# Kernel optimization log

Measured on AMD Instinct MI355X. Metric: run time of the kernel, lower is better.

Reference implementation:

```python
import jax, jax.numpy as jnp
import numpy as np

TOP_K = 2
NUM_EXPERTS = 8
ROUTE_SCALE = 1.0


def setup_inputs() -> dict:
    key = jax.random.key(0)
    ks = jax.random.split(key, 8)
    bs, slen, dim, hidden, E = 4, 1024, 2048, 1024, NUM_EXPERTS
    s = 0.02
    return {
        "x": jax.random.normal(ks[0], (bs, slen, dim), jnp.float32),
        "gate_w": jax.random.normal(ks[1], (E, dim), jnp.float32) * s,
        "w1": jax.random.normal(ks[2], (E, hidden, dim), jnp.float32) * s,
        "w2": jax.random.normal(ks[3], (E, dim, hidden), jnp.float32) * s,
        "w3": jax.random.normal(ks[4], (E, hidden, dim), jnp.float32) * s,
        "ws1": jax.random.normal(ks[5], (hidden, dim), jnp.float32) * s,
        "ws2": jax.random.normal(ks[6], (dim, hidden), jnp.float32) * s,
        "ws3": jax.random.normal(ks[7], (hidden, dim), jnp.float32) * s,
    }


def reference(x, gate_w, w1, w2, w3, ws1, ws2, ws3):
    bs, slen, dim = x.shape
    xf = x.reshape(-1, dim)  # (T, dim)
    # --- router: sigmoid scores in fp32, top-k (expert_bias is zeros at init) ---
    logits = (xf @ gate_w.T).astype(jnp.float32)  # (T, E)
    scores = jax.nn.sigmoid(logits)
    top_scores, sel_idx = jax.lax.top_k(scores, TOP_K)  # (T, k), (T, k)
    top_scores = top_scores * ROUTE_SCALE  # route_norm=False
    # --- routed experts: score_before_experts=True -> scale input by score ---
    routed = jnp.zeros_like(xf)
    for k in range(TOP_K):
        xs = xf * top_scores[:, k][:, None]  # (T, dim)
        h1 = jnp.einsum('td,ehd->teh', xs, w1)
        h3 = jnp.einsum('td,ehd->teh', xs, w3)
        h = jax.nn.silu(h1) * h3  # (T, E, hidden)
        onehot = jax.nn.one_hot(sel_idx[:, k], NUM_EXPERTS, dtype=h.dtype)  # (T, E)
        routed = routed + jnp.einsum('teh,te,edh->td', h, onehot, w2)
    # --- shared expert (SwiGLU FFN) ---
    shared = (jax.nn.silu(xf @ ws1.T) * (xf @ ws3.T)) @ ws2.T
    out = (shared + routed).reshape(bs, slen, dim)
    return out
```

## Files before the change

kernel.cpp:

```cpp
#include <hip/hip_runtime.h>
#include <hip/hip_bf16.h>
#include <cstdint>

#define TTOK   4096
#define DIM    2048
#define HID    1024
#define NEXP   8
#define GROWS  12288

typedef __attribute__((ext_vector_type(8))) __bf16 bf16x8;
typedef __attribute__((ext_vector_type(4))) float  f32x4;

__device__ __forceinline__ void glds16(const void* g, void* l) {
  __builtin_amdgcn_global_load_lds((const __attribute__((address_space(1))) void*)g,
                                   (__attribute__((address_space(3))) void*)l,
                                   16, 0, 0);
}

__global__ void convert_w(const float* __restrict__ w1, const float* __restrict__ w2,
                          const float* __restrict__ w3, const float* __restrict__ ws1,
                          const float* __restrict__ ws2, const float* __restrict__ ws3,
                          __bf16* __restrict__ w13, __bf16* __restrict__ w2c) {
  const int N1 = 9 * 2048 * 2048 / 8;
  const int N2 = 9 * 2048 * 1024 / 8;
  int s = blockIdx.x * 256 + threadIdx.x;
  const float* src;
  __bf16* dst;
  if (s < N1) {
    int e  = s / 524288;
    int r  = (s % 524288) / 256;
    int c  = (s % 256) * 8;
    if (r < 1024) src = (e < 8 ? w1 + ((size_t)e * 1024 + r) * 2048 : ws1 + (size_t)r * 2048) + c;
    else          src = (e < 8 ? w3 + ((size_t)e * 1024 + (r - 1024)) * 2048 : ws3 + (size_t)(r - 1024) * 2048) + c;
    dst = w13 + ((size_t)e * 2048 + r) * 2048 + c;
  } else {
    int s2 = s - N1;
    if (s2 >= N2) return;
    int e  = s2 / 262144;
    int r  = (s2 % 262144) / 128;
    int c  = (s2 % 128) * 8;
    src = (e < 8 ? w2 + ((size_t)e * 2048 + r) * 1024 : ws2 + (size_t)r * 1024) + c;
    dst = w2c + ((size_t)e * 2048 + r) * 1024 + c;
  }
  float4 a = *(const float4*)(src);
  float4 b = *(const float4*)(src + 4);
  bf16x8 o;
  o[0]=(__bf16)a.x; o[1]=(__bf16)a.y; o[2]=(__bf16)a.z; o[3]=(__bf16)a.w;
  o[4]=(__bf16)b.x; o[5]=(__bf16)b.y; o[6]=(__bf16)b.z; o[7]=(__bf16)b.w;
  *(bf16x8*)dst = o;
}

__global__ void router_k(const float* __restrict__ x, const float* __restrict__ gw,
                         int* __restrict__ sel, float* __restrict__ sco, int* __restrict__ counts) {
  int t    = blockIdx.x * 4 + (threadIdx.x >> 6);
  int lane = threadIdx.x & 63;
  const float* xr = x + (size_t)t * DIM;
  float acc[NEXP];
  #pragma unroll
  for (int e = 0; e < NEXP; ++e) acc[e] = 0.f;
  for (int d = lane * 4; d < DIM; d += 256) {
    float4 xv = *(const float4*)(xr + d);
    #pragma unroll
    for (int e = 0; e < NEXP; ++e) {
      float4 gv = *(const float4*)(gw + (size_t)e * DIM + d);
      acc[e] += xv.x * gv.x + xv.y * gv.y + xv.z * gv.z + xv.w * gv.w;
    }
  }
  #pragma unroll
  for (int off = 32; off; off >>= 1)
    #pragma unroll
    for (int e = 0; e < NEXP; ++e) acc[e] += __shfl_xor(acc[e], off);
  if (lane == 0) {
    float s[NEXP];
    #pragma unroll
    for (int e = 0; e < NEXP; ++e) s[e] = 1.f / (1.f + expf(-acc[e]));
    int e0 = 0;
    #pragma unroll
    for (int e = 1; e < NEXP; ++e) if (s[e] > s[e0]) e0 = e;
    int e1 = (e0 == 0) ? 1 : 0;
    #pragma unroll
    for (int e = 0; e < NEXP; ++e) if (e != e0 && s[e] > s[e1]) e1 = e;
    sel[2 * t] = e0; sel[2 * t + 1] = e1;
    sco[2 * t] = s[e0]; sco[2 * t + 1] = s[e1];
    atomicAdd(&counts[e0], 1); atomicAdd(&counts[e1], 1);
  }
}

__global__ void scan_k(const int* __restrict__ counts, int* __restrict__ offs) {
  if (threadIdx.x == 0 && blockIdx.x == 0) {
    int o = 0;
    for (int e = 0; e < NEXP; ++e) { offs[e] = o; o += counts[e]; }
    offs[NEXP] = o;
    offs[NEXP + 1] = o + TTOK;
  }
}

__global__ void gather_k(const float* __restrict__ x, const int* __restrict__ sel,
                         const float* __restrict__ sco, const int* __restrict__ offs,
                         int* __restrict__ cursor, int* __restrict__ token_rows,
                         __bf16* __restrict__ xg) {
  __shared__ int   rows[3];
  __shared__ float ss[3];
  int t = blockIdx.x;
  if (threadIdx.x == 0) {
    int e0 = sel[2 * t], e1 = sel[2 * t + 1];
    int r0 = offs[e0] + atomicAdd(&cursor[e0], 1);
    int r1 = offs[e1] + atomicAdd(&cursor[e1], 1);
    int r2 = 8192 + t;
    rows[0] = r0; rows[1] = r1; rows[2] = r2;
    ss[0] = sco[2 * t]; ss[1] = sco[2 * t + 1]; ss[2] = 1.0f;
    token_rows[3 * t] = r0; token_rows[3 * t + 1] = r1; token_rows[3 * t + 2] = r2;
  }
  __syncthreads();
  int c = threadIdx.x * 8;
  float4 v0 = *(const float4*)(x + (size_t)t * DIM + c);
  float4 v1 = *(const float4*)(x + (size_t)t * DIM + c + 4);
  #pragma unroll
  for (int j = 0; j < 3; ++j) {
    float s = ss[j];
    bf16x8 o;
    o[0]=(__bf16)(v0.x*s); o[1]=(__bf16)(v0.y*s); o[2]=(__bf16)(v0.z*s); o[3]=(__bf16)(v0.w*s);
    o[4]=(__bf16)(v1.x*s); o[5]=(__bf16)(v1.y*s); o[6]=(__bf16)(v1.z*s); o[7]=(__bf16)(v1.w*s);
    *(bf16x8*)(xg + (size_t)rows[j] * DIM + c) = o;
  }
}

template <int EPI>
__launch_bounds__(256)
__global__ void gemm_nt(const __bf16* __restrict__ A, const __bf16* __restrict__ Bw,
                        __bf16* __restrict__ Cb, float* __restrict__ c2a, float* __restrict__ c2b,
                        const int* __restrict__ offs, int K_, int N_) {
  int z  = blockIdx.z;
  int o0 = offs[z];
  int ne = offs[z + 1] - o0;

  int flat = blockIdx.y * 32 + blockIdx.x;
  int nid  = (flat & 7) * 64 + (flat >> 3);
  int bm   = nid & 31;
  int bn   = nid >> 5;

  if (bm * 128 >= ne) return;

  const __bf16* Aseg = A  + (size_t)(o0 + bm * 128) * K_;
  const __bf16* Bseg = Bw + ((size_t)z * N_ + bn * 128) * K_;

  __shared__ __align__(16) __bf16 sA[2][128 * 64];
  __shared__ __align__(16) __bf16 sB[2][128 * 64];

  int tid  = threadIdx.x;
  int wave = tid >> 6, lane = tid & 63;
  int wm = wave & 1, wn = wave >> 1;
  int fr = lane & 15;
  int fq = lane >> 4;
  int sw = fr & 7;

  f32x4 acc[4][4];
  #pragma unroll
  for (int i = 0; i < 4; ++i)
    #pragma unroll
    for (int j = 0; j < 4; ++j) acc[i][j] = (f32x4){0.f, 0.f, 0.f, 0.f};

#define STAGE(buf, kbase)                                                     \
  {                                                                           \
    _Pragma("unroll")                                                         \
    for (int it = 0; it < 4; ++it) {                                          \
      int s   = it * 256 + tid;                                               \
      int row = s >> 3;                                                       \
      int c8  = (s & 7) ^ (row & 7);                                          \
      glds16(Aseg + (size_t)row * K_ + (kbase) + c8 * 8, &sA[buf][s * 8]);    \
      glds16(Bseg + (size_t)row * K_ + (kbase) + c8 * 8, &sB[buf][s * 8]);    \
    }                                                                         \
  }

  STAGE(0, 0)
  __syncthreads();

  const int nk = K_ >> 6;
  for (int t = 0; t < nk; ++t) {
    int cur = t & 1;
    if (t + 1 < nk) STAGE(cur ^ 1, (t + 1) << 6)

    const __bf16* rAbase = &sA[cur][(wm * 64 + fr) * 64];
    const __bf16* rBbase = &sB[cur][(wn * 64 + fr) * 64];
    #pragma unroll
    for (int kk = 0; kk < 2; ++kk) {
      int slot = ((kk * 4 + fq) ^ sw) * 8;
      bf16x8 af[4], bb[4];
      #pragma unroll
      for (int i = 0; i < 4; ++i) af[i] = *(const bf16x8*)(rAbase + i * 16 * 64 + slot);
      #pragma unroll
      for (int i = 0; i < 4; ++i) bb[i] = *(const bf16x8*)(rBbase + i * 16 * 64 + slot);
      #pragma unroll
      for (int mi = 0; mi < 4; ++mi)
        #pragma unroll
        for (int ni = 0; ni < 4; ++ni)
          acc[mi][ni] = __builtin_amdgcn_mfma_f32_16x16x32_bf16(af[mi], bb[ni], acc[mi][ni], 0, 0, 0);
    }
    __syncthreads();
  }
#undef STAGE

  #pragma unroll
  for (int mi = 0; mi < 4; ++mi) {
    #pragma unroll
    for (int r = 0; r < 4; ++r) {
      int rl = bm * 128 + wm * 64 + mi * 16 + fq * 4 + r;
      if (rl < ne) {
        int grow = o0 + rl;
        if (EPI == 0) {
          size_t ro = (size_t)grow * 2048;
          #pragma unroll
          for (int ni = 0; ni < 4; ++ni) {
            int col = bn * 128 + wn * 64 + ni * 16 + fr;
            Cb[ro + col] = (__bf16)acc[mi][ni][r];
          }
        } else {
          float* dst = (grow < 8192) ? (c2a + (size_t)grow * 2048)
                                     : (c2b + (size_t)(grow - 8192) * 2048);
          #pragma unroll
          for (int ni = 0; ni < 4; ++ni) {
            int col = bn * 128 + wn * 64 + ni * 16 + fr;
            dst[col] = acc[mi][ni][r];
          }
        }
      }
    }
  }
}

__global__ void silu_mul(const __bf16* __restrict__ c13, __bf16* __restrict__ h) {
  int i   = blockIdx.x * 256 + threadIdx.x;
  int row = i >> 7;
  int c   = (i & 127) * 8;
  bf16x8 a = *(const bf16x8*)(c13 + (size_t)row * 2048 + c);
  bf16x8 b = *(const bf16x8*)(c13 + (size_t)row * 2048 + 1024 + c);
  bf16x8 o;
  #pragma unroll
  for (int j = 0; j < 8; ++j) {
    float xv = (float)a[j];
    float g  = xv / (1.f + expf(-xv));
    o[j] = (__bf16)(g * (float)b[j]);
  }
  *(bf16x8*)(h + (size_t)row * 1024 + c) = o;
}

__global__ void combine_k(const float* __restrict__ c2a, const float* __restrict__ c2b,
                          const int* __restrict__ token_rows, float* __restrict__ out) {
  __shared__ int rr[3];
  int t = blockIdx.x;
  if (threadIdx.x < 3) rr[threadIdx.x] = token_rows[3 * t + threadIdx.x];
  __syncthreads();
  int c = threadIdx.x * 8;
  const float* p0 = c2a + (size_t)rr[0] * 2048 + c;
  const float* p1 = c2a + (size_t)rr[1] * 2048 + c;
  const float* p2 = c2b + (size_t)(rr[2] - 8192) * 2048 + c;
  float4 a0 = *(const float4*)p0,       a1 = *(const float4*)p1,       a2 = *(const float4*)p2;
  float4 b0 = *(const float4*)(p0 + 4), b1 = *(const float4*)(p1 + 4), b2 = *(const float4*)(p2 + 4);
  float4 oa, ob;
  oa.x = a0.x + a1.x + a2.x; oa.y = a0.y + a1.y + a2.y;
  oa.z = a0.z + a1.z + a2.z; oa.w = a0.w + a1.w + a2.w;
  ob.x = b0.x + b1.x + b2.x; ob.y = b0.y + b1.y + b2.y;
  ob.z = b0.z + b1.z + b2.z; ob.w = b0.w + b1.w + b2.w;
  float* op = out + (size_t)t * 2048 + c;
  *(float4*)op = oa;
  *(float4*)(op + 4) = ob;
}

extern "C" void kernel_launch(void* const* d_in, const int* in_sizes, int n_in,
                              void* d_out, int out_size, void* d_ws, size_t ws_size,
                              hipStream_t stream) {
  const float* x   = (const float*)d_in[0];
  const float* gw  = (const float*)d_in[1];
  const float* w1  = (const float*)d_in[2];
  const float* w2  = (const float*)d_in[3];
  const float* w3  = (const float*)d_in[4];
  const float* ws1 = (const float*)d_in[5];
  const float* ws2 = (const float*)d_in[6];
  const float* ws3 = (const float*)d_in[7];
  float* out = (float*)d_out;

  char* p = (char*)d_ws;
  int*   counts     = (int*)p;
  int*   cursor     = (int*)(p + 64);
  int*   offs       = (int*)(p + 128);
  int*   sel        = (int*)(p + 1024);
  float* sco        = (float*)(p + 1024 + 32768);
  int*   token_rows = (int*)(p + 1024 + 65536);
  char* big = p + (1 << 20);
  __bf16* w13 = (__bf16*)big;
  __bf16* w2c = (__bf16*)(big + 75497472ull);
  __bf16* xg  = (__bf16*)(big + 75497472ull + 37748736ull);
  __bf16* c13 = (__bf16*)(big + 75497472ull + 37748736ull + 50331648ull);
  __bf16* hbuf = xg;
  float*  c2a  = (float*)w13;
  float*  c2b  = (float*)c13;

  hipMemsetAsync(p, 0, 256, stream);

  convert_w<<<27648, 256, 0, stream>>>(w1, w2, w3, ws1, ws2, ws3, w13, w2c);
  router_k<<<TTOK / 4, 256, 0, stream>>>(x, gw, sel, sco, counts);
  scan_k<<<1, 64, 0, stream>>>(counts, offs);
  gather_k<<<TTOK, 256, 0, stream>>>(x, sel, sco, offs, cursor, token_rows, xg);
  gemm_nt<0><<<dim3(32, 16, 9), 256, 0, stream>>>(xg, w13, c13, nullptr, nullptr, offs, 2048, 2048);
  silu_mul<<<GROWS * HID / 8 / 256, 256, 0, stream>>>(c13, hbuf);
  gemm_nt<1><<<dim3(32, 16, 9), 256, 0, stream>>>(hbuf, w2c, nullptr, c2a, c2b, offs, 1024, 2048);
  combine_k<<<TTOK, 256, 0, stream>>>(c2a, c2b, token_rows, out);
}
```

Measured before the change: 751.5 us.

## Fuse SiLU-mul into gate/up GEMM epilogue and enlarge GEMM tiles to 256x256

Interleaves the w1 and w3 rows in the converted weights so that adjacent output columns hold the h1/h3 pair, letting the first grouped GEMM compute silu(h1)*h3 in its epilogue with a lane shuffle and write the hidden activations directly. This removes the separate silu_mul kernel and the full bf16 round trip of the intermediate c13 buffer. The GEMM is also retiled to 256x256 blocks with 512 threads, explicit vmcnt waits, raw barriers and s_setprio around the MFMA bursts to overlap loads with compute. The larger tiles double LDS use and raise register pressure, and they halve the block count for experts with few rows. The extra barriers inside the inner loop may also cost time.

Measured after the change: 778.2 us. +3.5%, slower.

```diff
diff --git a/kernel.cpp b/kernel.cpp
--- a/kernel.cpp
+++ b/kernel.cpp
@@ -16,6 +16,9 @@
                                    (__attribute__((address_space(3))) void*)l,
                                    16, 0, 0);
 }
+
+#define BAR() do { asm volatile("" ::: "memory"); __builtin_amdgcn_s_barrier(); \
+                   asm volatile("" ::: "memory"); } while (0)
 
 __global__ void convert_w(const float* __restrict__ w1, const float* __restrict__ w2,
                           const float* __restrict__ w3, const float* __restrict__ ws1,
@@ -30,9 +33,12 @@
     int e  = s / 524288;
     int r  = (s % 524288) / 256;
     int c  = (s % 256) * 8;
-    if (r < 1024) src = (e < 8 ? w1 + ((size_t)e * 1024 + r) * 2048 : ws1 + (size_t)r * 2048) + c;
-    else          src = (e < 8 ? w3 + ((size_t)e * 1024 + (r - 1024)) * 2048 : ws3 + (size_t)(r - 1024) * 2048) + c;
-    dst = w13 + ((size_t)e * 2048 + r) * 2048 + c;
+    int nr;
+    if (r < 1024) { src = (e < 8 ? w1 + ((size_t)e * 1024 + r) * 2048 : ws1 + (size_t)r * 2048) + c;
+                    nr = 2 * r; }
+    else          { src = (e < 8 ? w3 + ((size_t)e * 1024 + (r - 1024)) * 2048 : ws3 + (size_t)(r - 1024) * 2048) + c;
+                    nr = 2 * (r - 1024) + 1; }
+    dst = w13 + ((size_t)e * 2048 + nr) * 2048 + c;
   } else {
     int s2 = s - N1;
     if (s2 >= N2) return;
@@ -126,37 +132,38 @@
 }
 
 template <int EPI>
-__launch_bounds__(256)
+__launch_bounds__(512, 2)
 __global__ void gemm_nt(const __bf16* __restrict__ A, const __bf16* __restrict__ Bw,
-                        __bf16* __restrict__ Cb, float* __restrict__ c2a, float* __restrict__ c2b,
+                        __bf16* __restrict__ Hb, float* __restrict__ c2a, float* __restrict__ c2b,
                         const int* __restrict__ offs, int K_, int N_) {
   int z  = blockIdx.z;
   int o0 = offs[z];
   int ne = offs[z + 1] - o0;
 
-  int flat = blockIdx.y * 32 + blockIdx.x;
-  int nid  = (flat & 7) * 64 + (flat >> 3);
-  int bm   = nid & 31;
-  int bn   = nid >> 5;
-
-  if (bm * 128 >= ne) return;
-
-  const __bf16* Aseg = A  + (size_t)(o0 + bm * 128) * K_;
-  const __bf16* Bseg = Bw + ((size_t)z * N_ + bn * 128) * K_;
-
-  __shared__ __align__(16) __bf16 sA[2][128 * 64];
-  __shared__ __align__(16) __bf16 sB[2][128 * 64];
+  int flat = blockIdx.y * 16 + blockIdx.x;
+  int nid  = (flat & 7) * 16 + (flat >> 3);
+  int bm   = nid & 15;
+  int bn   = nid >> 4;
+
+  if (bm * 256 >= ne) return;
+
+  const __bf16* Aseg = A  + (size_t)(o0 + bm * 256) * K_;
+  const __bf16* Bseg = Bw + ((size_t)z * N_ + bn * 256) * K_;
+
+  __shared__ __align__(16) __bf16 sA[2][256 * 64];
+  __shared__ __align__(16) __bf16 sB[2][256 * 64];
 
   int tid  = threadIdx.x;
   int wave = tid >> 6, lane = tid & 63;
-  int wm = wave & 1, wn = wave >> 1;
+  int wm = wave & 1;
+  int wn = wave >> 1;
   int fr = lane & 15;
   int fq = lane >> 4;
   int sw = fr & 7;
 
-  f32x4 acc[4][4];
-  #pragma unroll
-  for (int i = 0; i < 4; ++i)
+  f32x4 acc[8][4];
+  #pragma unroll
+  for (int i = 0; i < 8; ++i)
     #pragma unroll
     for (int j = 0; j < 4; ++j) acc[i][j] = (f32x4){0.f, 0.f, 0.f, 0.f};
 
@@ -164,7 +171,7 @@
   {                                                                           \
     _Pragma("unroll")                                                         \
     for (int it = 0; it < 4; ++it) {                                          \
-      int s   = it * 256 + tid;                                               \
+      int s   = it * 512 + tid;                                               \
       int row = s >> 3;                                                       \
       int c8  = (s & 7) ^ (row & 7);                                          \
       glds16(Aseg + (size_t)row * K_ + (kbase) + c8 * 8, &sA[buf][s * 8]);    \
@@ -173,75 +180,83 @@
   }
 
   STAGE(0, 0)
-  __syncthreads();
+  asm volatile("s_waitcnt vmcnt(0)" ::: "memory");
+  BAR();
 
   const int nk = K_ >> 6;
   for (int t = 0; t < nk; ++t) {
     int cur = t & 1;
-    if (t + 1 < nk) STAGE(cur ^ 1, (t + 1) << 6)
-
-    const __bf16* rAbase = &sA[cur][(wm * 64 + fr) * 64];
-    const __bf16* rBbase = &sB[cur][(wn * 64 + fr) * 64];
+    if (t + 1 < nk) {
+      STAGE(cur ^ 1, (t + 1) << 6)
+      asm volatile("s_waitcnt vmcnt(8)" ::: "memory");
+    } else {
+      asm volatile("s_waitcnt vmcnt(0)" ::: "memory");
+    }
+    BAR();
+
+    const __bf16* sAc = &sA[cur][0];
+    const __bf16* sBc = &sB[cur][0];
     #pragma unroll
     for (int kk = 0; kk < 2; ++kk) {
       int slot = ((kk * 4 + fq) ^ sw) * 8;
-      bf16x8 af[4], bb[4];
+      bf16x8 bb[4];
       #pragma unroll
-      for (int i = 0; i < 4; ++i) af[i] = *(const bf16x8*)(rAbase + i * 16 * 64 + slot);
+      for (int i = 0; i < 4; ++i)
+        bb[i] = *(const bf16x8*)(sBc + (wn * 64 + i * 16 + fr) * 64 + slot);
       #pragma unroll
-      for (int i = 0; i < 4; ++i) bb[i] = *(const bf16x8*)(rBbase + i * 16 * 64 + slot);
-      #pragma unroll
-      for (int mi = 0; mi < 4; ++mi)
+      for (int mh = 0; mh < 2; ++mh) {
+        bf16x8 af[4];
         #pragma unroll
-        for (int ni = 0; ni < 4; ++ni)
-          acc[mi][ni] = __builtin_amdgcn_mfma_f32_16x16x32_bf16(af[mi], bb[ni], acc[mi][ni], 0, 0, 0);
+        for (int i = 0; i < 4; ++i)
+          af[i] = *(const bf16x8*)(sAc + (wm * 128 + (mh * 4 + i) * 16 + fr) * 64 + slot);
+        BAR();
+        __builtin_amdgcn_s_setprio(1);
+        #pragma unroll
+        for (int i = 0; i < 4; ++i)
+          #pragma unroll
+          for (int j = 0; j < 4; ++j)
+            acc[mh * 4 + i][j] =
+                __builtin_amdgcn_mfma_f32_16x16x32_bf16(af[i], bb[j], acc[mh * 4 + i][j], 0, 0, 0);
+        __builtin_amdgcn_s_setprio(0);
+        BAR();
+      }
     }
-    __syncthreads();
   }
 #undef STAGE
 
   #pragma unroll
-  for (int mi = 0; mi < 4; ++mi) {
+  for (int mi = 0; mi < 8; ++mi) {
     #pragma unroll
     for (int r = 0; r < 4; ++r) {
-      int rl = bm * 128 + wm * 64 + mi * 16 + fq * 4 + r;
-      if (rl < ne) {
-        int grow = o0 + rl;
-        if (EPI == 0) {
-          size_t ro = (size_t)grow * 2048;
-          #pragma unroll
-          for (int ni = 0; ni < 4; ++ni) {
-            int col = bn * 128 + wn * 64 + ni * 16 + fr;
-            Cb[ro + col] = (__bf16)acc[mi][ni][r];
+      int rl = bm * 256 + wm * 128 + mi * 16 + fq * 4 + r;
+      bool ok = rl < ne;
+      int grow = o0 + rl;
+      if (EPI == 0) {
+        #pragma unroll
+        for (int ni = 0; ni < 4; ++ni) {
+          float v = acc[mi][ni][r];
+          float o = __shfl_xor(v, 1);
+          float h1 = (fr & 1) ? o : v;
+          float h3 = (fr & 1) ? v : o;
+          float g  = h1 / (1.f + expf(-h1)) * h3;
+          if (ok && !(fr & 1)) {
+            int hcol = bn * 128 + wn * 32 + ni * 8 + (fr >> 1);
+            Hb[(size_t)grow * 1024 + hcol] = (__bf16)g;
           }
-        } else {
+        }
+      } else {
+        if (ok) {
           float* dst = (grow < 8192) ? (c2a + (size_t)grow * 2048)
                                      : (c2b + (size_t)(grow - 8192) * 2048);
           #pragma unroll
           for (int ni = 0; ni < 4; ++ni) {
-            int col = bn * 128 + wn * 64 + ni * 16 + fr;
+            int col = bn * 256 + wn * 64 + ni * 16 + fr;
             dst[col] = acc[mi][ni][r];
           }
         }
       }
     }
   }
-}
-
-__global__ void silu_mul(const __bf16* __restrict__ c13, __bf16* __restrict__ h) {
-  int i   = blockIdx.x * 256 + threadIdx.x;
-  int row = i >> 7;
-  int c   = (i & 127) * 8;
-  bf16x8 a = *(const bf16x8*)(c13 + (size_t)row * 2048 + c);
-  bf16x8 b = *(const bf16x8*)(c13 + (size_t)row * 2048 + 1024 + c);
-  bf16x8 o;
-  #pragma unroll
-  for (int j = 0; j < 8; ++j) {
-    float xv = (float)a[j];
-    float g  = xv / (1.f + expf(-xv));
-    o[j] = (__bf16)(g * (float)b[j]);
-  }
-  *(bf16x8*)(h + (size_t)row * 1024 + c) = o;
 }
 
 __global__ void combine_k(const float* __restrict__ c2a, const float* __restrict__ c2b,
@@ -287,13 +302,12 @@
   float* sco        = (float*)(p + 1024 + 32768);
   int*   token_rows = (int*)(p + 1024 + 65536);
   char* big = p + (1 << 20);
-  __bf16* w13 = (__bf16*)big;
-  __bf16* w2c = (__bf16*)(big + 75497472ull);
-  __bf16* xg  = (__bf16*)(big + 75497472ull + 37748736ull);
-  __bf16* c13 = (__bf16*)(big + 75497472ull + 37748736ull + 50331648ull);
-  __bf16* hbuf = xg;
+  __bf16* w13  = (__bf16*)big;
+  __bf16* w2c  = (__bf16*)(big + 75497472ull);
+  __bf16* xg   = (__bf16*)(big + 75497472ull + 37748736ull);
+  __bf16* hbuf = (__bf16*)(big + 75497472ull + 37748736ull + 50331648ull);
   float*  c2a  = (float*)w13;
-  float*  c2b  = (float*)c13;
+  float*  c2b  = (float*)xg;
 
   hipMemsetAsync(p, 0, 256, stream);
 
@@ -301,8 +315,7 @@
   router_k<<<TTOK / 4, 256, 0, stream>>>(x, gw, sel, sco, counts);
   scan_k<<<1, 64, 0, stream>>>(counts, offs);
   gather_k<<<TTOK, 256, 0, stream>>>(x, sel, sco, offs, cursor, token_rows, xg);
-  gemm_nt<0><<<dim3(32, 16, 9), 256, 0, stream>>>(xg, w13, c13, nullptr, nullptr, offs, 2048, 2048);
-  silu_mul<<<GROWS * HID / 8 / 256, 256, 0, stream>>>(c13, hbuf);
-  gemm_nt<1><<<dim3(32, 16, 9), 256, 0, stream>>>(hbuf, w2c, nullptr, c2a, c2b, offs, 1024, 2048);
+  gemm_nt<0><<<dim3(16, 8, 9), 512, 0, stream>>>(xg, w13, hbuf, nullptr, nullptr, offs, 2048, 2048);
+  gemm_nt<1><<<dim3(16, 8, 9), 512, 0, stream>>>(hbuf, w2c, nullptr, c2a, c2b, offs, 1024, 2048);
   combine_k<<<TTOK, 256, 0, stream>>>(c2a, c2b, token_rows, out);
 }
```

## Fuse SiLU-mul into gate/up GEMM epilogue via interleaved w1/w3 rows

Applied to the files above, without the earlier changes.

The weight conversion now interleaves w1 and w3 rows, so each adjacent pair of output columns in the first grouped GEMM holds matching h1 and h3 values. The epilogue swaps them with a lane shuffle, applies SiLU times gate, and writes the bf16 hidden activations directly. This removes the separate silu_mul pass and its bf16 c13 round trip through memory. Weight conversion and the router are also merged into a single launch to cut one kernel launch. In exchange, half the lanes issue scattered 2-byte stores, and c2b is now aliased onto xg, so buffer-reuse correctness depends on xg holding at least 4096 fp32 rows of 2048.

New measurement: 741.6 us. No clear change (-1.3%).

```diff
diff --git a/kernel.cpp b/kernel.cpp
--- a/kernel.cpp
+++ b/kernel.cpp
@@ -17,42 +17,49 @@
                                    16, 0, 0);
 }
 
-__global__ void convert_w(const float* __restrict__ w1, const float* __restrict__ w2,
-                          const float* __restrict__ w3, const float* __restrict__ ws1,
-                          const float* __restrict__ ws2, const float* __restrict__ ws3,
-                          __bf16* __restrict__ w13, __bf16* __restrict__ w2c) {
+__global__ void convert_router_k(const float* __restrict__ w1, const float* __restrict__ w2,
+                                 const float* __restrict__ w3, const float* __restrict__ ws1,
+                                 const float* __restrict__ ws2, const float* __restrict__ ws3,
+                                 __bf16* __restrict__ w13, __bf16* __restrict__ w2c,
+                                 const float* __restrict__ x, const float* __restrict__ gw,
+                                 int* __restrict__ sel, float* __restrict__ sco,
+                                 int* __restrict__ counts) {
   const int N1 = 9 * 2048 * 2048 / 8;
   const int N2 = 9 * 2048 * 1024 / 8;
-  int s = blockIdx.x * 256 + threadIdx.x;
-  const float* src;
-  __bf16* dst;
-  if (s < N1) {
-    int e  = s / 524288;
-    int r  = (s % 524288) / 256;
-    int c  = (s % 256) * 8;
-    if (r < 1024) src = (e < 8 ? w1 + ((size_t)e * 1024 + r) * 2048 : ws1 + (size_t)r * 2048) + c;
-    else          src = (e < 8 ? w3 + ((size_t)e * 1024 + (r - 1024)) * 2048 : ws3 + (size_t)(r - 1024) * 2048) + c;
-    dst = w13 + ((size_t)e * 2048 + r) * 2048 + c;
-  } else {
-    int s2 = s - N1;
-    if (s2 >= N2) return;
-    int e  = s2 / 262144;
-    int r  = (s2 % 262144) / 128;
-    int c  = (s2 % 128) * 8;
-    src = (e < 8 ? w2 + ((size_t)e * 2048 + r) * 1024 : ws2 + (size_t)r * 1024) + c;
-    dst = w2c + ((size_t)e * 2048 + r) * 1024 + c;
-  }
-  float4 a = *(const float4*)(src);
-  float4 b = *(const float4*)(src + 4);
-  bf16x8 o;
-  o[0]=(__bf16)a.x; o[1]=(__bf16)a.y; o[2]=(__bf16)a.z; o[3]=(__bf16)a.w;
-  o[4]=(__bf16)b.x; o[5]=(__bf16)b.y; o[6]=(__bf16)b.z; o[7]=(__bf16)b.w;
-  *(bf16x8*)dst = o;
-}
-
-__global__ void router_k(const float* __restrict__ x, const float* __restrict__ gw,
-                         int* __restrict__ sel, float* __restrict__ sco, int* __restrict__ counts) {
-  int t    = blockIdx.x * 4 + (threadIdx.x >> 6);
+  const int CONV_BLOCKS = (N1 + N2) / 256;
+
+  if (blockIdx.x < (unsigned)CONV_BLOCKS) {
+    int s = blockIdx.x * 256 + threadIdx.x;
+    const float* src;
+    __bf16* dst;
+    if (s < N1) {
+      int e  = s / 524288;
+      int r  = (s % 524288) / 256;
+      int c  = (s % 256) * 8;
+      int nr;
+      if (r < 1024) { src = (e < 8 ? w1 + ((size_t)e * 1024 + r) * 2048 : ws1 + (size_t)r * 2048) + c;
+                      nr = 2 * r; }
+      else          { src = (e < 8 ? w3 + ((size_t)e * 1024 + (r - 1024)) * 2048 : ws3 + (size_t)(r - 1024) * 2048) + c;
+                      nr = 2 * (r - 1024) + 1; }
+      dst = w13 + ((size_t)e * 2048 + nr) * 2048 + c;
+    } else {
+      int s2 = s - N1;
+      int e  = s2 / 262144;
+      int r  = (s2 % 262144) / 128;
+      int c  = (s2 % 128) * 8;
+      src = (e < 8 ? w2 + ((size_t)e * 2048 + r) * 1024 : ws2 + (size_t)r * 1024) + c;
+      dst = w2c + ((size_t)e * 2048 + r) * 1024 + c;
+    }
+    float4 a = *(const float4*)(src);
+    float4 b = *(const float4*)(src + 4);
+    bf16x8 o;
+    o[0]=(__bf16)a.x; o[1]=(__bf16)a.y; o[2]=(__bf16)a.z; o[3]=(__bf16)a.w;
+    o[4]=(__bf16)b.x; o[5]=(__bf16)b.y; o[6]=(__bf16)b.z; o[7]=(__bf16)b.w;
+    *(bf16x8*)dst = o;
+    return;
+  }
+
+  int t    = (blockIdx.x - CONV_BLOCKS) * 4 + (threadIdx.x >> 6);
   int lane = threadIdx.x & 63;
   const float* xr = x + (size_t)t * DIM;
   float acc[NEXP];
@@ -128,7 +135,7 @@
 template <int EPI>
 __launch_bounds__(256)
 __global__ void gemm_nt(const __bf16* __restrict__ A, const __bf16* __restrict__ Bw,
-                        __bf16* __restrict__ Cb, float* __restrict__ c2a, float* __restrict__ c2b,
+                        __bf16* __restrict__ Hb, float* __restrict__ c2a, float* __restrict__ c2b,
                         const int* __restrict__ offs, int K_, int N_) {
   int z  = blockIdx.z;
   int o0 = offs[z];
@@ -205,16 +212,23 @@
     #pragma unroll
     for (int r = 0; r < 4; ++r) {
       int rl = bm * 128 + wm * 64 + mi * 16 + fq * 4 + r;
-      if (rl < ne) {
-        int grow = o0 + rl;
-        if (EPI == 0) {
-          size_t ro = (size_t)grow * 2048;
-          #pragma unroll
-          for (int ni = 0; ni < 4; ++ni) {
-            int col = bn * 128 + wn * 64 + ni * 16 + fr;
-            Cb[ro + col] = (__bf16)acc[mi][ni][r];
+      bool ok = rl < ne;
+      int grow = o0 + rl;
+      if (EPI == 0) {
+        #pragma unroll
+        for (int ni = 0; ni < 4; ++ni) {
+          float v = acc[mi][ni][r];
+          float o = __shfl_xor(v, 1);
+          float h1 = (fr & 1) ? o : v;
+          float h3 = (fr & 1) ? v : o;
+          float g  = h1 / (1.f + expf(-h1)) * h3;
+          if (ok && !(fr & 1)) {
+            int hcol = bn * 64 + wn * 32 + ni * 8 + (fr >> 1);
+            Hb[(size_t)grow * 1024 + hcol] = (__bf16)g;
           }
-        } else {
+        }
+      } else {
+        if (ok) {
           float* dst = (grow < 8192) ? (c2a + (size_t)grow * 2048)
                                      : (c2b + (size_t)(grow - 8192) * 2048);
           #pragma unroll
@@ -226,22 +240,6 @@
       }
     }
   }
-}
-
-__global__ void silu_mul(const __bf16* __restrict__ c13, __bf16* __restrict__ h) {
-  int i   = blockIdx.x * 256 + threadIdx.x;
-  int row = i >> 7;
-  int c   = (i & 127) * 8;
-  bf16x8 a = *(const bf16x8*)(c13 + (size_t)row * 2048 + c);
-  bf16x8 b = *(const bf16x8*)(c13 + (size_t)row * 2048 + 1024 + c);
-  bf16x8 o;
-  #pragma unroll
-  for (int j = 0; j < 8; ++j) {
-    float xv = (float)a[j];
-    float g  = xv / (1.f + expf(-xv));
-    o[j] = (__bf16)(g * (float)b[j]);
-  }
-  *(bf16x8*)(h + (size_t)row * 1024 + c) = o;
 }
 
 __global__ void combine_k(const float* __restrict__ c2a, const float* __restrict__ c2b,
@@ -287,22 +285,20 @@
   float* sco        = (float*)(p + 1024 + 32768);
   int*   token_rows = (int*)(p + 1024 + 65536);
   char* big = p + (1 << 20);
-  __bf16* w13 = (__bf16*)big;
-  __bf16* w2c = (__bf16*)(big + 75497472ull);
-  __bf16* xg  = (__bf16*)(big + 75497472ull + 37748736ull);
-  __bf16* c13 = (__bf16*)(big + 75497472ull + 37748736ull + 50331648ull);
-  __bf16* hbuf = xg;
+  __bf16* w13  = (__bf16*)big;
+  __bf16* w2c  = (__bf16*)(big + 75497472ull);
+  __bf16* xg   = (__bf16*)(big + 75497472ull + 37748736ull);
+  __bf16* hbuf = (__bf16*)(big + 75497472ull + 37748736ull + 50331648ull);
   float*  c2a  = (float*)w13;
-  float*  c2b  = (float*)c13;
+  float*  c2b  = (float*)xg;
 
   hipMemsetAsync(p, 0, 256, stream);
 
-  convert_w<<<27648, 256, 0, stream>>>(w1, w2, w3, ws1, ws2, ws3, w13, w2c);
-  router_k<<<TTOK / 4, 256, 0, stream>>>(x, gw, sel, sco, counts);
+  convert_router_k<<<27648 + TTOK / 4, 256, 0, stream>>>(w1, w2, w3, ws1, ws2, ws3, w13, w2c,
+                                                         x, gw, sel, sco, counts);
   scan_k<<<1, 64, 0, stream>>>(counts, offs);
   gather_k<<<TTOK, 256, 0, stream>>>(x, sel, sco, offs, cursor, token_rows, xg);
-  gemm_nt<0><<<dim3(32, 16, 9), 256, 0, stream>>>(xg, w13, c13, nullptr, nullptr, offs, 2048, 2048);
-  silu_mul<<<GROWS * HID / 8 / 256, 256, 0, stream>>>(c13, hbuf);
+  gemm_nt<0><<<dim3(32, 16, 9), 256, 0, stream>>>(xg, w13, hbuf, nullptr, nullptr, offs, 2048, 2048);
   gemm_nt<1><<<dim3(32, 16, 9), 256, 0, stream>>>(hbuf, w2c, nullptr, c2a, c2b, offs, 1024, 2048);
   combine_k<<<TTOK, 256, 0, stream>>>(c2a, c2b, token_rows, out);
 }
```
